# Performance work log

Hardware: AMD Instinct MI355X
Metric: run time of the kernel (lower is better)

## Reference

```python
import jax, jax.numpy as jnp
import numpy as np

IN_DIM = 2048
OUT_DIM = 2048
BATCH = 4096

def _xavier(key, fan_in, fan_out):
    std = np.sqrt(2.0 / (fan_in + fan_out)).astype(np.float32)
    return jax.random.normal(key, (fan_in, fan_out), dtype=jnp.float32) * std

def setup_inputs() -> dict:
    key = jax.random.key(0)
    ks = jax.random.split(key, 12)
    inp = {
        'X': jax.random.normal(ks[0], (BATCH, IN_DIM), dtype=jnp.float32),
        'C': jax.random.normal(ks[1], (BATCH, OUT_DIM), dtype=jnp.float32),
        'H': jax.random.normal(ks[2], (BATCH, OUT_DIM), dtype=jnp.float32),
        'W_xf': _xavier(ks[3], IN_DIM, OUT_DIM),
        'W_xg': _xavier(ks[4], IN_DIM, OUT_DIM),
        'W_xi': _xavier(ks[5], IN_DIM, OUT_DIM),
        'W_xo': _xavier(ks[6], IN_DIM, OUT_DIM),
        'W_hf': _xavier(ks[7], OUT_DIM, OUT_DIM),
        'W_hg': _xavier(ks[8], OUT_DIM, OUT_DIM),
        'W_hi': _xavier(ks[9], OUT_DIM, OUT_DIM),
        'W_ho': _xavier(ks[10], OUT_DIM, OUT_DIM),
        'b_f': jnp.zeros((1, OUT_DIM), dtype=jnp.float32),
        'b_g': jnp.zeros((1, OUT_DIM), dtype=jnp.float32),
        'b_i': jnp.zeros((1, OUT_DIM), dtype=jnp.float32),
        'b_o': jnp.zeros((1, OUT_DIM), dtype=jnp.float32),
    }
    return inp

def reference(X, C, H, W_xf, W_xg, W_xi, W_xo, W_hf, W_hg, W_hi, W_ho, b_f, b_g, b_i, b_o):
    # LSTM cell: 4 gates, each x@W_x* + b_* + h@W_h*
    F = jax.nn.sigmoid(X @ W_xf + b_f + H @ W_hf)
    I = jax.nn.sigmoid(X @ W_xi + b_i + H @ W_hi)
    O = jax.nn.sigmoid(X @ W_xo + b_o + H @ W_ho)
    G = jnp.tanh(X @ W_xg + b_g + H @ W_hg)
    C_new = G * I + F * C
    Y = O * jnp.tanh(C_new)
    return (C_new, Y)
```

## Files before the change

kernel.cpp:

```cpp
#include <hip/hip_runtime.h>
#include <cstdint>
#include <cstddef>

#define BATCH   4096
#define IN_DIM  2048
#define OUT_DIM 2048
#define KDIM    4096

typedef __bf16 bf16x8 __attribute__((ext_vector_type(8)));
typedef float  floatx4 __attribute__((ext_vector_type(4)));

__device__ __forceinline__ unsigned short f2bf(float f) {
  unsigned int u = __float_as_uint(f);
  u += 0x7FFFu + ((u >> 16) & 1u);
  return (unsigned short)(u >> 16);
}

__device__ __forceinline__ void async16(const void* g, void* l) {
  __builtin_amdgcn_global_load_lds(
      (const __attribute__((address_space(1))) unsigned int*)g,
      (__attribute__((address_space(3))) unsigned int*)l, 16, 0, 0);
}

__device__ __forceinline__ float tanh_fast(float x) {
  return 1.f - 2.f / (__expf(2.f * x) + 1.f);
}

__global__ __launch_bounds__(256) void pack_A_kernel(
    const float* __restrict__ X, const float* __restrict__ H,
    unsigned short* __restrict__ A) {
  int idx = blockIdx.x * 256 + threadIdx.x;
  int e = idx << 2;
  int m = e >> 12;
  int k = e & 4095;
  const float* src = (k < IN_DIM) ? (X + (size_t)m * IN_DIM + k)
                                  : (H + (size_t)m * OUT_DIM + (k - IN_DIM));
  float4 v = *(const float4*)src;
  ushort4 o;
  o.x = f2bf(v.x); o.y = f2bf(v.y); o.z = f2bf(v.z); o.w = f2bf(v.w);
  *(ushort4*)(A + e) = o;
}

__global__ __launch_bounds__(256) void pack_B_kernel(
    const float* __restrict__ Wxf, const float* __restrict__ Wxi,
    const float* __restrict__ Wxo, const float* __restrict__ Wxg,
    const float* __restrict__ Whf, const float* __restrict__ Whi,
    const float* __restrict__ Who, const float* __restrict__ Whg,
    unsigned short* __restrict__ Bt) {
  __shared__ float tile[64][33];
  int bx = blockIdx.x;
  int kT = bx & 63;
  int nT = bx >> 6;
  int k0 = kT * 64, n0 = nT * 32;
  int g = n0 >> 11;
  int c0 = n0 & 2047;
  const float* W;
  int kk0;
  if (k0 < IN_DIM) {
    kk0 = k0;
    W = (g == 0) ? Wxf : (g == 1) ? Wxi : (g == 2) ? Wxo : Wxg;
  } else {
    kk0 = k0 - IN_DIM;
    W = (g == 0) ? Whf : (g == 1) ? Whi : (g == 2) ? Who : Whg;
  }
  int t = threadIdx.x;
#pragma unroll
  for (int i = 0; i < 2; ++i) {
    int idx = i * 256 + t;
    int lk = idx >> 3, lc = (idx & 7) * 4;
    float4 v = *(const float4*)(W + (size_t)(kk0 + lk) * 2048 + c0 + lc);
    tile[lk][lc]     = v.x;
    tile[lk][lc + 1] = v.y;
    tile[lk][lc + 2] = v.z;
    tile[lk][lc + 3] = v.w;
  }
  __syncthreads();
  int ln = t >> 3, k8 = (t & 7) * 8;
  unsigned int p[4];
#pragma unroll
  for (int j = 0; j < 4; ++j) {
    unsigned int lo = f2bf(tile[k8 + 2 * j][ln]);
    unsigned int hi = f2bf(tile[k8 + 2 * j + 1][ln]);
    p[j] = lo | (hi << 16);
  }
  uint4 o = make_uint4(p[0], p[1], p[2], p[3]);
  *(uint4*)(Bt + (size_t)(n0 + ln) * KDIM + k0 + k8) = o;
}

__global__ __launch_bounds__(256, 2) void lstm_gemm_fused(
    const unsigned short* __restrict__ A,
    const unsigned short* __restrict__ Bt,
    const float* __restrict__ Cin,
    const float* __restrict__ bF, const float* __restrict__ bI,
    const float* __restrict__ bO, const float* __restrict__ bG,
    float* __restrict__ outC, float* __restrict__ outY) {
  __shared__ unsigned short lA[256 * 32];
  __shared__ unsigned short lB[128 * 32];

  const int t = threadIdx.x;
  const int lane = t & 63;
  const int w = t >> 6;
  const int mBase = blockIdx.y * 256;
  const int nBase = blockIdx.x * 32;

  floatx4 acc[4][2][4];
#pragma unroll
  for (int g = 0; g < 4; ++g)
#pragma unroll
    for (int nf = 0; nf < 2; ++nf)
#pragma unroll
      for (int mt = 0; mt < 4; ++mt) acc[g][nf][mt] = (floatx4){0.f, 0.f, 0.f, 0.f};

  const int rowT = t >> 2;
  const int cswz = (((t & 3) ^ ((t >> 3) & 3))) * 16;
  const char* aG = (const char*)(A + (size_t)(mBase + rowT) * KDIM) + cswz;
  const size_t aStep = (size_t)64 * KDIM * 2;
  const int r1 = 64 + rowT;
  const char* bG0 = (const char*)(Bt + (size_t)((rowT >> 5) * 2048 + nBase + (rowT & 31)) * KDIM) + cswz;
  const char* bG1 = (const char*)(Bt + (size_t)((r1 >> 5) * 2048 + nBase + (r1 & 31)) * KDIM) + cswz;
  char* lAdst = (char*)lA + t * 16;
  char* lBdst = (char*)lB + t * 16;

  const int fr = lane & 15;
  const int fk = lane >> 4;
  const int fkx = fk ^ ((fr >> 1) & 3);

  for (int k0 = 0; k0 < KDIM; k0 += 32) {
    const int kb = k0 * 2;
    async16(aG + kb,             lAdst);
    async16(aG + kb + aStep,     lAdst + 4096);
    async16(aG + kb + 2 * aStep, lAdst + 8192);
    async16(aG + kb + 3 * aStep, lAdst + 12288);
    async16(bG0 + kb,            lBdst);
    async16(bG1 + kb,            lBdst + 4096);
    __syncthreads();

    const bf16x8* A8 = (const bf16x8*)lA;
    const bf16x8* B8 = (const bf16x8*)lB;
    bf16x8 af[4], bfrag[8];
#pragma unroll
    for (int mt = 0; mt < 4; ++mt)
      af[mt] = A8[(w * 64 + mt * 16 + fr) * 4 + fkx];
#pragma unroll
    for (int g = 0; g < 4; ++g)
#pragma unroll
      for (int nf = 0; nf < 2; ++nf)
        bfrag[g * 2 + nf] = B8[(g * 32 + nf * 16 + fr) * 4 + fkx];
#pragma unroll
    for (int g = 0; g < 4; ++g)
#pragma unroll
      for (int nf = 0; nf < 2; ++nf)
#pragma unroll
        for (int mt = 0; mt < 4; ++mt)
          acc[g][nf][mt] = __builtin_amdgcn_mfma_f32_16x16x32_bf16(
              af[mt], bfrag[g * 2 + nf], acc[g][nf][mt], 0, 0, 0);
    __syncthreads();
  }

  const int col0 = nBase + (lane & 15);
  const int rb = mBase + w * 64 + (lane >> 4) * 4;
#pragma unroll
  for (int nf = 0; nf < 2; ++nf) {
    const int col = col0 + nf * 16;
    const float bfv = bF[col], biv = bI[col], bov = bO[col], bgv = bG[col];
#pragma unroll
    for (int mt = 0; mt < 4; ++mt) {
#pragma unroll
      for (int r = 0; r < 4; ++r) {
        const int row = rb + mt * 16 + r;
        const size_t off = (size_t)row * OUT_DIM + col;
        float pf = acc[0][nf][mt][r] + bfv;
        float pi = acc[1][nf][mt][r] + biv;
        float po = acc[2][nf][mt][r] + bov;
        float pg = acc[3][nf][mt][r] + bgv;
        float F = 1.f / (1.f + __expf(-pf));
        float I = 1.f / (1.f + __expf(-pi));
        float O = 1.f / (1.f + __expf(-po));
        float G = tanh_fast(pg);
        float c_new = G * I + F * Cin[off];
        outC[off] = c_new;
        outY[off] = O * tanh_fast(c_new);
      }
    }
  }
}

extern "C" void kernel_launch(void* const* d_in, const int* in_sizes, int n_in,
                              void* d_out, int out_size, void* d_ws, size_t ws_size,
                              hipStream_t stream) {
  const float* X   = (const float*)d_in[0];
  const float* C   = (const float*)d_in[1];
  const float* H   = (const float*)d_in[2];
  const float* Wxf = (const float*)d_in[3];
  const float* Wxg = (const float*)d_in[4];
  const float* Wxi = (const float*)d_in[5];
  const float* Wxo = (const float*)d_in[6];
  const float* Whf = (const float*)d_in[7];
  const float* Whg = (const float*)d_in[8];
  const float* Whi = (const float*)d_in[9];
  const float* Who = (const float*)d_in[10];
  const float* bf_ = (const float*)d_in[11];
  const float* bg_ = (const float*)d_in[12];
  const float* bi_ = (const float*)d_in[13];
  const float* bo_ = (const float*)d_in[14];

  float* outC = (float*)d_out;
  float* outY = (float*)d_out + (size_t)BATCH * OUT_DIM;

  unsigned short* A  = (unsigned short*)d_ws;
  unsigned short* Bt = A + (size_t)BATCH * KDIM;

  pack_A_kernel<<<(BATCH * KDIM / 4) / 256, 256, 0, stream>>>(X, H, A);
  pack_B_kernel<<<64 * 256, 256, 0, stream>>>(Wxf, Wxi, Wxo, Wxg,
                                              Whf, Whi, Who, Whg, Bt);
  dim3 grid(OUT_DIM / 32, BATCH / 256);
  lstm_gemm_fused<<<grid, 256, 0, stream>>>(A, Bt, C, bf_, bi_, bo_, bg_,
                                            outC, outY);
}
```

Baseline: 540.4 us.

## Double-buffer LDS tiles to overlap global loads with MFMA compute

Splits the A and B shared-memory tiles into two buffers and prefetches the next K-slice into the idle buffer while MFMAs run on the current one. This drops one barrier per iteration and hides global-to-LDS latency. It also raises wave priority around the MFMA block with s_setprio. LDS use doubles to 48KB per block, which may reduce how many blocks fit per CU. Correctness depends on the async LDS writes finishing before the single barrier at the end of each iteration.

```diff
diff --git a/kernel.cpp b/kernel.cpp
--- a/kernel.cpp
+++ b/kernel.cpp
@@ -6,6 +6,7 @@
 #define IN_DIM  2048
 #define OUT_DIM 2048
 #define KDIM    4096
+#define NT      128
 
 typedef __bf16 bf16x8 __attribute__((ext_vector_type(8)));
 typedef float  floatx4 __attribute__((ext_vector_type(4)));
@@ -94,8 +95,8 @@
     const float* __restrict__ bF, const float* __restrict__ bI,
     const float* __restrict__ bO, const float* __restrict__ bG,
     float* __restrict__ outC, float* __restrict__ outY) {
-  __shared__ unsigned short lA[256 * 32];
-  __shared__ unsigned short lB[128 * 32];
+  __shared__ unsigned short lA[2][256 * 32];
+  __shared__ unsigned short lB[2][128 * 32];
 
   const int t = threadIdx.x;
   const int lane = t & 63;
@@ -118,25 +119,36 @@
   const int r1 = 64 + rowT;
   const char* bG0 = (const char*)(Bt + (size_t)((rowT >> 5) * 2048 + nBase + (rowT & 31)) * KDIM) + cswz;
   const char* bG1 = (const char*)(Bt + (size_t)((r1 >> 5) * 2048 + nBase + (r1 & 31)) * KDIM) + cswz;
-  char* lAdst = (char*)lA + t * 16;
-  char* lBdst = (char*)lB + t * 16;
+  char* lAd = (char*)lA + t * 16;
+  char* lBd = (char*)lB + t * 16;
 
   const int fr = lane & 15;
   const int fk = lane >> 4;
   const int fkx = fk ^ ((fr >> 1) & 3);
 
-  for (int k0 = 0; k0 < KDIM; k0 += 32) {
-    const int kb = k0 * 2;
-    async16(aG + kb,             lAdst);
-    async16(aG + kb + aStep,     lAdst + 4096);
-    async16(aG + kb + 2 * aStep, lAdst + 8192);
-    async16(aG + kb + 3 * aStep, lAdst + 12288);
-    async16(bG0 + kb,            lBdst);
-    async16(bG1 + kb,            lBdst + 4096);
-    __syncthreads();
-
-    const bf16x8* A8 = (const bf16x8*)lA;
-    const bf16x8* B8 = (const bf16x8*)lB;
+  {
+    async16(aG,             lAd);
+    async16(aG + aStep,     lAd + 4096);
+    async16(aG + 2 * aStep, lAd + 8192);
+    async16(aG + 3 * aStep, lAd + 12288);
+    async16(bG0,            lBd);
+    async16(bG1,            lBd + 4096);
+  }
+  __syncthreads();
+
+  for (int kt = 0; kt < NT; ++kt) {
+    const int cur = kt & 1, nxt = cur ^ 1;
+    if (kt + 1 < NT) {
+      const int kb = (kt + 1) * 64;
+      async16(aG + kb,             lAd + nxt * 16384);
+      async16(aG + kb + aStep,     lAd + nxt * 16384 + 4096);
+      async16(aG + kb + 2 * aStep, lAd + nxt * 16384 + 8192);
+      async16(aG + kb + 3 * aStep, lAd + nxt * 16384 + 12288);
+      async16(bG0 + kb,            lBd + nxt * 8192);
+      async16(bG1 + kb,            lBd + nxt * 8192 + 4096);
+    }
+    const bf16x8* A8 = (const bf16x8*)lA[cur];
+    const bf16x8* B8 = (const bf16x8*)lB[cur];
     bf16x8 af[4], bfrag[8];
 #pragma unroll
     for (int mt = 0; mt < 4; ++mt)
@@ -146,6 +158,7 @@
 #pragma unroll
       for (int nf = 0; nf < 2; ++nf)
         bfrag[g * 2 + nf] = B8[(g * 32 + nf * 16 + fr) * 4 + fkx];
+    __builtin_amdgcn_s_setprio(1);
 #pragma unroll
     for (int g = 0; g < 4; ++g)
 #pragma unroll
@@ -154,6 +167,7 @@
         for (int mt = 0; mt < 4; ++mt)
           acc[g][nf][mt] = __builtin_amdgcn_mfma_f32_16x16x32_bf16(
               af[mt], bfrag[g * 2 + nf], acc[g][nf][mt], 0, 0, 0);
+    __builtin_amdgcn_s_setprio(0);
     __syncthreads();
   }
 
```

After: 547.8 us. Within noise of the previous version (+1.4%).

## Double-buffer LDS pipeline with 512-thread blocks and larger N tile for fused LSTM GEMM

Applied to the files above, without the earlier changes.

Rewrites the fused GEMM main loop around two 32 KB LDS stages. Async global-to-LDS loads for the next K tiles are issued between MFMA phases, and manual vmcnt waits and barriers replace the two __syncthreads per iteration. Each workgroup grows to 512 threads covering 256 rows by 64 columns per gate, with 2x4 waves, plus a remapped block order for L2 locality and s_setprio around MFMA bursts. This is meant to hide global-load latency and raise arithmetic intensity per LDS byte, at the cost of more LDS (64 KB per block), lower occupancy, and fragile hand-written waitcnt counts.

```diff
diff --git a/kernel.cpp b/kernel.cpp
--- a/kernel.cpp
+++ b/kernel.cpp
@@ -6,6 +6,7 @@
 #define IN_DIM  2048
 #define OUT_DIM 2048
 #define KDIM    4096
+#define NT      128
 
 typedef __bf16 bf16x8 __attribute__((ext_vector_type(8)));
 typedef float  floatx4 __attribute__((ext_vector_type(4)));
@@ -87,100 +88,146 @@
   *(uint4*)(Bt + (size_t)(n0 + ln) * KDIM + k0 + k8) = o;
 }
 
-__global__ __launch_bounds__(256, 2) void lstm_gemm_fused(
+template <bool LAST, bool IG1, bool IG2>
+__device__ __forceinline__ void do_tile(
+    const char* sl, char* sn,
+    const char* aG_1, const char* aG_2, const char* bG_1, const char* bG_2,
+    unsigned kbG1, unsigned kbG2, int t16,
+    int aOffA, int bOff, floatx4 (&acc)[4][8]) {
+  bf16x8 af[4], bfr[4];
+  if (LAST) asm volatile("s_waitcnt vmcnt(1)" ::: "memory");
+  else      asm volatile("s_waitcnt vmcnt(4)" ::: "memory");
+  asm volatile("s_barrier" ::: "memory");
+#pragma unroll
+  for (int mt = 0; mt < 4; ++mt)
+    af[mt] = *(const bf16x8*)(sl + aOffA + mt * 1024);
+#pragma unroll
+  for (int nf = 0; nf < 4; ++nf)
+    bfr[nf] = *(const bf16x8*)(sl + bOff + nf * 4096);
+  if (IG2) async16(aG_2 + kbG2, sn + 8192 + t16);
+  __builtin_amdgcn_s_setprio(1);
+#pragma unroll
+  for (int nf = 0; nf < 4; ++nf)
+#pragma unroll
+    for (int mt = 0; mt < 4; ++mt)
+      acc[nf][mt] = __builtin_amdgcn_mfma_f32_16x16x32_bf16(
+          af[mt], bfr[nf], acc[nf][mt], 0, 0, 0);
+  __builtin_amdgcn_s_setprio(0);
+  if (LAST) asm volatile("s_waitcnt vmcnt(0)" ::: "memory");
+  else      asm volatile("s_waitcnt vmcnt(4)" ::: "memory");
+  asm volatile("s_barrier" ::: "memory");
+#pragma unroll
+  for (int mt = 0; mt < 4; ++mt)
+    af[mt] = *(const bf16x8*)(sl + aOffA + 8192 + mt * 1024);
+  if (IG1) {
+    char* sc = const_cast<char*>(sl);
+    async16(aG_1 + kbG1, sc + t16);
+    async16(bG_1 + kbG1, sc + 16384 + t16);
+    async16(bG_2 + kbG1, sc + 24576 + t16);
+  }
+  __builtin_amdgcn_s_setprio(1);
+#pragma unroll
+  for (int nf = 0; nf < 4; ++nf)
+#pragma unroll
+    for (int mt = 0; mt < 4; ++mt)
+      acc[nf][mt + 4] = __builtin_amdgcn_mfma_f32_16x16x32_bf16(
+          af[mt], bfr[nf], acc[nf][mt + 4], 0, 0, 0);
+  __builtin_amdgcn_s_setprio(0);
+}
+
+__global__ __launch_bounds__(512, 2) void lstm_gemm_fused(
     const unsigned short* __restrict__ A,
     const unsigned short* __restrict__ Bt,
     const float* __restrict__ Cin,
     const float* __restrict__ bF, const float* __restrict__ bI,
     const float* __restrict__ bO, const float* __restrict__ bG,
     float* __restrict__ outC, float* __restrict__ outY) {
-  __shared__ unsigned short lA[256 * 32];
-  __shared__ unsigned short lB[128 * 32];
+  __shared__ __align__(16) char smem[65536];
 
   const int t = threadIdx.x;
   const int lane = t & 63;
   const int w = t >> 6;
-  const int mBase = blockIdx.y * 256;
-  const int nBase = blockIdx.x * 32;
-
-  floatx4 acc[4][2][4];
+  const int wm = w >> 2;
+  const int wn = w & 3;
+
+  const int orig = blockIdx.x;
+  const int wgid = (orig & 7) * 64 + (orig >> 3);
+  const int bx = wgid & 31;
+  const int by = wgid >> 5;
+  const int mBase = by * 256;
+
+  floatx4 acc[4][8];
 #pragma unroll
   for (int g = 0; g < 4; ++g)
 #pragma unroll
-    for (int nf = 0; nf < 2; ++nf)
-#pragma unroll
-      for (int mt = 0; mt < 4; ++mt) acc[g][nf][mt] = (floatx4){0.f, 0.f, 0.f, 0.f};
+    for (int mt = 0; mt < 8; ++mt) acc[g][mt] = (floatx4){0.f, 0.f, 0.f, 0.f};
 
   const int rowT = t >> 2;
-  const int cswz = (((t & 3) ^ ((t >> 3) & 3))) * 16;
-  const char* aG = (const char*)(A + (size_t)(mBase + rowT) * KDIM) + cswz;
-  const size_t aStep = (size_t)64 * KDIM * 2;
-  const int r1 = 64 + rowT;
-  const char* bG0 = (const char*)(Bt + (size_t)((rowT >> 5) * 2048 + nBase + (rowT & 31)) * KDIM) + cswz;
-  const char* bG1 = (const char*)(Bt + (size_t)((r1 >> 5) * 2048 + nBase + (r1 & 31)) * KDIM) + cswz;
-  char* lAdst = (char*)lA + t * 16;
-  char* lBdst = (char*)lB + t * 16;
+  const int cswz = ((t & 3) ^ ((t >> 3) & 3)) * 16;
+  const int physA = rowT + (rowT & 64);
+  const char* aG_1 = (const char*)A + ((size_t)(mBase + physA) * KDIM) * 2 + cswz;
+  const char* aG_2 = aG_1 + (size_t)64 * KDIM * 2;
+  const int bRow = (rowT >> 6) * 2048 + bx * 64 + (rowT & 63);
+  const char* bG_1 = (const char*)Bt + ((size_t)bRow * KDIM) * 2 + cswz;
+  const char* bG_2 = bG_1 + (size_t)4096 * KDIM * 2;
+  const int t16 = t * 16;
 
   const int fr = lane & 15;
-  const int fk = lane >> 4;
-  const int fkx = fk ^ ((fr >> 1) & 3);
-
-  for (int k0 = 0; k0 < KDIM; k0 += 32) {
-    const int kb = k0 * 2;
-    async16(aG + kb,             lAdst);
-    async16(aG + kb + aStep,     lAdst + 4096);
-    async16(aG + kb + 2 * aStep, lAdst + 8192);
-    async16(aG + kb + 3 * aStep, lAdst + 12288);
-    async16(bG0 + kb,            lBdst);
-    async16(bG1 + kb,            lBdst + 4096);
-    __syncthreads();
-
-    const bf16x8* A8 = (const bf16x8*)lA;
-    const bf16x8* B8 = (const bf16x8*)lB;
-    bf16x8 af[4], bfrag[8];
-#pragma unroll
-    for (int mt = 0; mt < 4; ++mt)
-      af[mt] = A8[(w * 64 + mt * 16 + fr) * 4 + fkx];
-#pragma unroll
-    for (int g = 0; g < 4; ++g)
-#pragma unroll
-      for (int nf = 0; nf < 2; ++nf)
-        bfrag[g * 2 + nf] = B8[(g * 32 + nf * 16 + fr) * 4 + fkx];
-#pragma unroll
-    for (int g = 0; g < 4; ++g)
-#pragma unroll
-      for (int nf = 0; nf < 2; ++nf)
-#pragma unroll
-        for (int mt = 0; mt < 4; ++mt)
-          acc[g][nf][mt] = __builtin_amdgcn_mfma_f32_16x16x32_bf16(
-              af[mt], bfrag[g * 2 + nf], acc[g][nf][mt], 0, 0, 0);
-    __syncthreads();
-  }
-
-  const int col0 = nBase + (lane & 15);
-  const int rb = mBase + w * 64 + (lane >> 4) * 4;
-#pragma unroll
-  for (int nf = 0; nf < 2; ++nf) {
-    const int col = col0 + nf * 16;
-    const float bfv = bF[col], biv = bI[col], bov = bO[col], bgv = bG[col];
-#pragma unroll
-    for (int mt = 0; mt < 4; ++mt) {
-#pragma unroll
-      for (int r = 0; r < 4; ++r) {
-        const int row = rb + mt * 16 + r;
-        const size_t off = (size_t)row * OUT_DIM + col;
-        float pf = acc[0][nf][mt][r] + bfv;
-        float pi = acc[1][nf][mt][r] + biv;
-        float po = acc[2][nf][mt][r] + bov;
-        float pg = acc[3][nf][mt][r] + bgv;
-        float F = 1.f / (1.f + __expf(-pf));
-        float I = 1.f / (1.f + __expf(-pi));
-        float O = 1.f / (1.f + __expf(-po));
-        float G = tanh_fast(pg);
-        float c_new = G * I + F * Cin[off];
-        outC[off] = c_new;
-        outY[off] = O * tanh_fast(c_new);
-      }
+  const int fkxB = (((lane >> 4) ^ ((fr >> 1) & 3))) * 16;
+  const int aOffA = (wm * 64 + fr) * 64 + fkxB;
+  const int bOff = 16384 + (wn * 16 + fr) * 64 + fkxB;
+
+  async16(aG_1,      smem + t16);
+  async16(bG_1,      smem + 16384 + t16);
+  async16(bG_2,      smem + 24576 + t16);
+  async16(aG_2,      smem + 8192 + t16);
+  async16(aG_1 + 64, smem + 32768 + t16);
+  async16(bG_1 + 64, smem + 32768 + 16384 + t16);
+  async16(bG_2 + 64, smem + 32768 + 24576 + t16);
+
+  for (int tt = 0; tt < NT - 2; ++tt) {
+    const char* sl = smem + (tt & 1) * 32768;
+    char* sn = smem + ((tt + 1) & 1) * 32768;
+    do_tile<false, true, true>(sl, sn, aG_1, aG_2, bG_1, bG_2,
+                               (unsigned)(tt + 2) * 64, (unsigned)(tt + 1) * 64,
+                               t16, aOffA, bOff, acc);
+  }
+  {
+    const int tt = NT - 2;
+    const char* sl = smem + (tt & 1) * 32768;
+    char* sn = smem + ((tt + 1) & 1) * 32768;
+    do_tile<false, false, true>(sl, sn, aG_1, aG_2, bG_1, bG_2,
+                                0, (unsigned)(tt + 1) * 64,
+                                t16, aOffA, bOff, acc);
+  }
+  {
+    const int tt = NT - 1;
+    const char* sl = smem + (tt & 1) * 32768;
+    char* sn = smem + ((tt + 1) & 1) * 32768;
+    do_tile<true, false, false>(sl, sn, aG_1, aG_2, bG_1, bG_2,
+                                0, 0, t16, aOffA, bOff, acc);
+  }
+
+  const int col = bx * 64 + wn * 16 + fr;
+  const float bfv = bF[col], biv = bI[col], bov = bO[col], bgv = bG[col];
+  const int rb = mBase + wm * 128 + ((lane >> 4) << 2);
+#pragma unroll
+  for (int mt = 0; mt < 8; ++mt) {
+#pragma unroll
+    for (int r = 0; r < 4; ++r) {
+      const int row = rb + mt * 16 + r;
+      const size_t off = (size_t)row * OUT_DIM + col;
+      float pf = acc[0][mt][r] + bfv;
+      float pi = acc[1][mt][r] + biv;
+      float po = acc[2][mt][r] + bov;
+      float pg = acc[3][mt][r] + bgv;
+      float F = 1.f / (1.f + __expf(-pf));
+      float I = 1.f / (1.f + __expf(-pi));
+      float O = 1.f / (1.f + __expf(-po));
+      float G = tanh_fast(pg);
+      float c_new = G * I + F * Cin[off];
+      outC[off] = c_new;
+      outY[off] = O * tanh_fast(c_new);
     }
   }
 }
@@ -213,7 +260,6 @@
   pack_A_kernel<<<(BATCH * KDIM / 4) / 256, 256, 0, stream>>>(X, H, A);
   pack_B_kernel<<<64 * 256, 256, 0, stream>>>(Wxf, Wxi, Wxo, Wxg,
                                               Whf, Whi, Who, Whg, Bt);
-  dim3 grid(OUT_DIM / 32, BATCH / 256);
-  lstm_gemm_fused<<<grid, 256, 0, stream>>>(A, Bt, C, bf_, bi_, bo_, bg_,
-                                            outC, outY);
-}
+  lstm_gemm_fused<<<dim3(512), dim3(512), 0, stream>>>(
+      A, Bt, C, bf_, bi_, bo_, bg_, outC, outY);
+}
```

Measured after the change: 525.8 us. -2.7%, faster.
